# Kernel optimization log

Measured on AMD Instinct MI355X. Metric: run time of the kernel, lower is better.

The kernel has to match this reference:

```python
import jax, jax.numpy as jnp
from jax import lax
import numpy as np

B, T, F_IN, H = 64, 128, 12, 128  # batch, seq_len, input/output features, hidden


def _uinit(key, shape, fan):
    return jax.random.uniform(key, shape, jnp.float32, -1.0, 1.0) / np.float32(np.sqrt(fan))


def setup_inputs() -> dict:
    key = jax.random.key(0)
    ks = jax.random.split(key, 12)
    inp = {
        "x": jax.random.normal(ks[0], (B, T, F_IN), jnp.float32),
        # encoder LSTM (gate order i,f,g,o; b = b_ih + b_hh folded together)
        "enc_Wih": _uinit(ks[1], (4 * H, F_IN), H),
        "enc_Whh": _uinit(ks[2], (4 * H, H), H),
        "enc_b": _uinit(ks[3], (4 * H,), H),
        # decoder LSTM (input is the 12-dim teacher-forced x slice)
        "dec_Wih": _uinit(ks[4], (4 * H, F_IN), H),
        "dec_Whh": _uinit(ks[5], (4 * H, H), H),
        "dec_b": _uinit(ks[6], (4 * H,), H),
        # attention: Linear(2H -> H) with bias, then v: Linear(H -> 1, no bias)
        "attn_W": _uinit(ks[7], (H, 2 * H), 2 * H),
        "attn_b": _uinit(ks[8], (H,), 2 * H),
        "v_w": _uinit(ks[9], (H,), H),
        # output layer: Linear(2H -> F_IN)  (intended width; see notes)
        "out_W": _uinit(ks[10], (F_IN, 2 * H), 2 * H),
        "out_b": _uinit(ks[11], (F_IN,), 2 * H),
    }
    return inp


def _lstm_cell(xt, h, c, Wih, Whh, b):
    z = xt @ Wih.T + h @ Whh.T + b  # [B, 4H]
    i, f, g, o = jnp.split(z, 4, axis=-1)
    c = jax.nn.sigmoid(f) * c + jax.nn.sigmoid(i) * jnp.tanh(g)
    h = jax.nn.sigmoid(o) * jnp.tanh(c)
    return h, c


def reference(x, enc_Wih, enc_Whh, enc_b, dec_Wih, dec_Whh, dec_b,
              attn_W, attn_b, v_w, out_W, out_b):
    b_, t_, _ = x.shape
    hdim = enc_Whh.shape[1]
    xs = jnp.swapaxes(x, 0, 1)  # [T, B, F]
    h0 = jnp.zeros((b_, hdim), x.dtype)
    c0 = jnp.zeros((b_, hdim), x.dtype)

    def enc_step(carry, xt):
        h, c = carry
        h, c = _lstm_cell(xt, h, c, enc_Wih, enc_Whh, enc_b)
        return (h, c), h

    (hT, cT), enc_hs = lax.scan(enc_step, (h0, c0), xs)
    enc_out = jnp.swapaxes(enc_hs, 0, 1)  # [B, T, H]

    # split attn weight: cat(hidden, enc_out) @ W.T == hidden@W1.T + enc_out@W2.T
    W1, W2 = attn_W[:, :hdim], attn_W[:, hdim:]
    enc_proj = jnp.einsum("bth,gh->btg", enc_out, W2)  # precompute encoder side

    def dec_step(carry, xt):
        h, c = carry
        h, c = _lstm_cell(xt, h, c, dec_Wih, dec_Whh, dec_b)
        energy = jnp.tanh((h @ W1.T)[:, None, :] + enc_proj + attn_b)  # [B,T,H]
        score = jnp.einsum("bth,h->bt", energy, v_w)
        w = jax.nn.softmax(score, axis=1)  # attention over encoder time
        ctx = jnp.einsum("bt,bth->bh", w, enc_out)
        return (h, c), jnp.concatenate([h, ctx], axis=-1)  # [B, 2H]

    _, dec_ys = lax.scan(dec_step, (hT, cT), xs)
    dec_out = jnp.swapaxes(dec_ys, 0, 1)  # [B, T, 2H]
    return dec_out @ out_W.T + out_b  # [B, T, F]
```

## Files before the change

kernel.cpp:

```cpp
#include <hip/hip_runtime.h>
#include <hip/hip_bf16.h>

#define BB 64
#define TT 128
#define FIN 12
#define HH 128
#define GG 512

#define LOG2E 1.4426950408889634f
#define TWO_LOG2E 2.8853900817779268f

__device__ __forceinline__ float fexp2(float x) { return __builtin_amdgcn_exp2f(x); }
__device__ __forceinline__ float frcp(float x)  { return __builtin_amdgcn_rcpf(x); }

__device__ __forceinline__ float tanh_f(float x) {
  return 1.0f - 2.0f * frcp(1.0f + fexp2(TWO_LOG2E * x));
}
__device__ __forceinline__ float sigm_f(float x) {
  return frcp(1.0f + fexp2(-LOG2E * x));
}

template <int CTRL>
__device__ __forceinline__ float dpp_addstage(float v) {
  int s = __builtin_amdgcn_update_dpp(0, __float_as_int(v), CTRL, 0xF, 0xF, true);
  return v + __int_as_float(s);
}
__device__ __forceinline__ float red8(float v) {
  v = dpp_addstage<0xB1>(v);
  v = dpp_addstage<0x4E>(v);
  v = dpp_addstage<0x141>(v);
  return v;
}

#define FMA4S(acc, s, v) do { \
  acc.x = fmaf((s), (v).x, acc.x); \
  acc.y = fmaf((s), (v).y, acc.y); \
  acc.z = fmaf((s), (v).z, acc.z); \
  acc.w = fmaf((s), (v).w, acc.w); } while (0)

#define ACC4(hv, wv, a) do { \
  a = fmaf((hv).x, (wv).x, a); a = fmaf((hv).y, (wv).y, a); \
  a = fmaf((hv).z, (wv).z, a); a = fmaf((hv).w, (wv).w, a); } while (0)

__global__ __launch_bounds__(1024, 4) void lstm_kernel(
    const float* __restrict__ x,
    const float* __restrict__ eWih, const float* __restrict__ eWhh, const float* __restrict__ eb,
    const float* __restrict__ dWih, const float* __restrict__ dWhh, const float* __restrict__ db,
    float* __restrict__ encH, float* __restrict__ decH)
{
  const int b   = blockIdx.x;
  const int tid = threadIdx.x;
  const int q   = tid & 7;
  const int i   = tid >> 3;

  __shared__ __align__(16) float xs[TT * FIN];
  __shared__ __align__(16) float hbuf[2][160];
  __shared__ __align__(16) float hist[64 * HH];

  if (tid < (TT * FIN / 4))
    ((float4*)xs)[tid] = ((const float4*)(x + (size_t)b * TT * FIN))[tid];
  if (tid < 320) ((float*)hbuf)[tid] = 0.0f;
  float c = 0.0f;

  const int xo   = (q < 4) ? 3 * q : 0;
  const float xz = (q < 4) ? 1.0f : 0.0f;

  int ts = 0;
  #pragma unroll 1
  for (int phase = 0; phase < 2; ++phase) {
    const float* Wih  = phase ? dWih : eWih;
    const float* Whh  = phase ? dWhh : eWhh;
    const float* bias = phase ? db : eb;
    float* Hout       = phase ? decH : encH;

    float4 wg[4][4];
    #pragma unroll
    for (int g = 0; g < 4; ++g)
      #pragma unroll
      for (int j = 0; j < 4; ++j)
        wg[g][j] = *(const float4*)(Whh + ((g * HH + i) * HH) + 16 * q + 4 * j);

    float wx[4][3];
    #pragma unroll
    for (int g = 0; g < 4; ++g)
      #pragma unroll
      for (int j = 0; j < 3; ++j)
        wx[g][j] = Wih[(g * HH + i) * FIN + xo + j] * xz;

    const float bi = bias[i], bf = bias[HH + i], bg = bias[2 * HH + i], bo = bias[3 * HH + i];

    #pragma unroll 1
    for (int half = 0; half < 2; ++half) {
      #pragma unroll 1
      for (int tt = 0; tt < 64; ++tt, ++ts) {
        const int t = half * 64 + tt;
        __syncthreads();
        const float* hb = hbuf[ts & 1] + q * 20;
        float4 h0 = *(const float4*)(hb + 0);
        float4 h1 = *(const float4*)(hb + 4);
        float4 h2 = *(const float4*)(hb + 8);
        float4 h3 = *(const float4*)(hb + 12);

        const float* xt = xs + t * FIN + xo;
        float x0 = xt[0], x1 = xt[1], x2 = xt[2];
        float ai = wx[0][0] * x0 + wx[0][1] * x1 + wx[0][2] * x2;
        float af = wx[1][0] * x0 + wx[1][1] * x1 + wx[1][2] * x2;
        float ag = wx[2][0] * x0 + wx[2][1] * x1 + wx[2][2] * x2;
        float ao = wx[3][0] * x0 + wx[3][1] * x1 + wx[3][2] * x2;

        ACC4(h0, wg[0][0], ai); ACC4(h0, wg[1][0], af); ACC4(h0, wg[2][0], ag); ACC4(h0, wg[3][0], ao);
        ACC4(h1, wg[0][1], ai); ACC4(h1, wg[1][1], af); ACC4(h1, wg[2][1], ag); ACC4(h1, wg[3][1], ao);
        ACC4(h2, wg[0][2], ai); ACC4(h2, wg[1][2], af); ACC4(h2, wg[2][2], ag); ACC4(h2, wg[3][2], ao);
        ACC4(h3, wg[0][3], ai); ACC4(h3, wg[1][3], af); ACC4(h3, wg[2][3], ag); ACC4(h3, wg[3][3], ao);

        ai = red8(ai); af = red8(af); ag = red8(ag); ao = red8(ao);

        if (q == 0) {
          float zi = sigm_f(ai + bi);
          float zf = sigm_f(af + bf);
          float zg = tanh_f(ag + bg);
          float zo = sigm_f(ao + bo);
          c = fmaf(zf, c, zi * zg);
          float hn = zo * tanh_f(c);
          hbuf[(ts + 1) & 1][(i >> 4) * 20 + (i & 15)] = hn;
          hist[tt * HH + i] = hn;
        }
      }
      __syncthreads();
      {
        float4* dst = (float4*)(Hout + ((size_t)b * TT + half * 64) * HH);
        const float4* src = (const float4*)hist;
        dst[tid]        = src[tid];
        dst[tid + 1024] = src[tid + 1024];
      }
    }
  }
}

__global__ __launch_bounds__(256, 2) void proj_kernel(
    const float* __restrict__ encH, const float* __restrict__ decH,
    const float* __restrict__ attnW, const float* __restrict__ attnb,
    float* __restrict__ Abuf, float* __restrict__ Pbuf)
{
  const int m  = blockIdx.x & 1;
  const int b  = (blockIdx.x >> 1) & 63;
  const int r0 = (blockIdx.x >> 7) * 16;
  const int tid = threadIdx.x;

  __shared__ __align__(16) float WT[64 * 128];
  __shared__ __align__(16) float Xt[16 * 128];

  const float* X = (m ? encH : decH) + ((size_t)b * TT + r0) * HH;
  const float* W = attnW + (m ? HH : 0);

  ((float4*)Xt)[tid]       = ((const float4*)X)[tid];
  ((float4*)Xt)[256 + tid] = ((const float4*)X)[256 + tid];

  const int hq = tid & 31, rr = tid >> 5;
  const int h0 = 4 * hq;

  float4 acc0, acc1;
  if (m == 0) { acc0 = *(const float4*)(attnb + h0); acc1 = acc0; }
  else        { acc0 = make_float4(0.f, 0.f, 0.f, 0.f); acc1 = acc0; }

  for (int kb = 0; kb < 2; ++kb) {
    __syncthreads();
    {
      int h = tid >> 1, koff = (tid & 1) * 32;
      #pragma unroll
      for (int j = 0; j < 8; ++j) {
        float4 v = *(const float4*)(W + h * 256 + kb * 64 + koff + 4 * j);
        int kp = koff + 4 * j;
        WT[(kp + 0) * 128 + h] = v.x;
        WT[(kp + 1) * 128 + h] = v.y;
        WT[(kp + 2) * 128 + h] = v.z;
        WT[(kp + 3) * 128 + h] = v.w;
      }
    }
    __syncthreads();
    const float* xr0 = Xt + (2 * rr) * 128 + kb * 64;
    const float* xr1 = xr0 + 128;
    #pragma unroll
    for (int k4 = 0; k4 < 64; k4 += 4) {
      float4 xa = *(const float4*)(xr0 + k4);
      float4 xb = *(const float4*)(xr1 + k4);
      float4 w0 = *(const float4*)&WT[(k4 + 0) * 128 + h0];
      float4 w1 = *(const float4*)&WT[(k4 + 1) * 128 + h0];
      float4 w2 = *(const float4*)&WT[(k4 + 2) * 128 + h0];
      float4 w3 = *(const float4*)&WT[(k4 + 3) * 128 + h0];
      FMA4S(acc0, xa.x, w0); FMA4S(acc0, xa.y, w1);
      FMA4S(acc0, xa.z, w2); FMA4S(acc0, xa.w, w3);
      FMA4S(acc1, xb.x, w0); FMA4S(acc1, xb.y, w1);
      FMA4S(acc1, xb.z, w2); FMA4S(acc1, xb.w, w3);
    }
  }
  float* O = (m ? Pbuf : Abuf) + ((size_t)b * TT + r0) * HH;
  *(float4*)(O + (2 * rr) * 128 + h0)     = acc0;
  *(float4*)(O + (2 * rr + 1) * 128 + h0) = acc1;
}

#define AST 132

__global__ __launch_bounds__(512, 2) void attn_kernel(
    const float* __restrict__ encH, const float* __restrict__ decH,
    const float* __restrict__ Abuf, const float* __restrict__ Pbuf,
    const float* __restrict__ vw, const float* __restrict__ outW,
    const float* __restrict__ outb, float* __restrict__ out)
{
  const int b  = blockIdx.x >> 3;
  const int s0 = (blockIdx.x & 7) * 16;
  const int tid = threadIdx.x;

  __shared__ __align__(16) float buf[64 * 128];
  __shared__ __align__(16) float a_lds[16 * AST];
  __shared__ __align__(16) float sc[16 * AST];
  __shared__ __align__(16) float dh[16 * 128];
  __shared__ __align__(16) float vl[HH];

  {
    int r = tid >> 5, c4 = (tid & 31) * 4;
    float4 av = *(const float4*)(Abuf + ((size_t)b * TT + s0 + r) * HH + c4);
    av.x = fexp2(TWO_LOG2E * av.x);
    av.y = fexp2(TWO_LOG2E * av.y);
    av.z = fexp2(TWO_LOG2E * av.z);
    av.w = fexp2(TWO_LOG2E * av.w);
    *(float4*)&a_lds[r * AST + c4] = av;
  }
  ((float4*)dh)[tid] = ((const float4*)(decH + ((size_t)b * TT + s0) * HH))[tid];
  if (tid < 32) ((float4*)vl)[tid] = ((const float4*)vw)[tid];

  const int u  = tid & 31;
  const int sl = tid >> 5;
  const int uq = u & 15;
  const int uh = u >> 4;

  for (int half = 0; half < 2; ++half) {
    const int tbase = half * 64;
    __syncthreads();
    #pragma unroll
    for (int i = 0; i < 4; ++i) {
      int flat = i * 2048 + tid * 4;
      int tp = flat >> 7;
      int h0 = flat & 127;
      float4 v = *(const float4*)(Pbuf + ((size_t)b * TT + tbase + tp) * HH + h0);
      v.x = fexp2(TWO_LOG2E * v.x);
      v.y = fexp2(TWO_LOG2E * v.y);
      v.z = fexp2(TWO_LOG2E * v.z);
      v.w = fexp2(TWO_LOG2E * v.w);
      int tq = tp >> 2, tr = tp & 3;
      buf[(h0 + 0) * 64 + 4 * ((tq ^ ((h0 + 0) >> 2)) & 15) + tr] = v.x;
      buf[(h0 + 1) * 64 + 4 * ((tq ^ ((h0 + 1) >> 2)) & 15) + tr] = v.y;
      buf[(h0 + 2) * 64 + 4 * ((tq ^ ((h0 + 2) >> 2)) & 15) + tr] = v.z;
      buf[(h0 + 3) * 64 + 4 * ((tq ^ ((h0 + 3) >> 2)) & 15) + tr] = v.w;
    }
    __syncthreads();
    float4 acc = make_float4(0.f, 0.f, 0.f, 0.f);
    const float* earow = a_lds + sl * AST;
    #pragma unroll 4
    for (int hh = 0; hh < 64; hh += 4) {
      const int h = uh * 64 + hh;
      float4 ea = *(const float4*)&earow[h];
      float4 va = *(const float4*)&vl[h];
      const int xoff = 4 * ((uq ^ ((h >> 2) & 15)) & 15);
      float4 p0 = *(const float4*)&buf[(h + 0) * 64 + xoff];
      float4 p1 = *(const float4*)&buf[(h + 1) * 64 + xoff];
      float4 p2 = *(const float4*)&buf[(h + 2) * 64 + xoff];
      float4 p3 = *(const float4*)&buf[(h + 3) * 64 + xoff];
      acc.x = fmaf(va.x, frcp(fmaf(ea.x, p0.x, 1.f)), acc.x);
      acc.y = fmaf(va.x, frcp(fmaf(ea.x, p0.y, 1.f)), acc.y);
      acc.z = fmaf(va.x, frcp(fmaf(ea.x, p0.z, 1.f)), acc.z);
      acc.w = fmaf(va.x, frcp(fmaf(ea.x, p0.w, 1.f)), acc.w);
      acc.x = fmaf(va.y, frcp(fmaf(ea.y, p1.x, 1.f)), acc.x);
      acc.y = fmaf(va.y, frcp(fmaf(ea.y, p1.y, 1.f)), acc.y);
      acc.z = fmaf(va.y, frcp(fmaf(ea.y, p1.z, 1.f)), acc.z);
      acc.w = fmaf(va.y, frcp(fmaf(ea.y, p1.w, 1.f)), acc.w);
      acc.x = fmaf(va.z, frcp(fmaf(ea.z, p2.x, 1.f)), acc.x);
      acc.y = fmaf(va.z, frcp(fmaf(ea.z, p2.y, 1.f)), acc.y);
      acc.z = fmaf(va.z, frcp(fmaf(ea.z, p2.z, 1.f)), acc.z);
      acc.w = fmaf(va.z, frcp(fmaf(ea.z, p2.w, 1.f)), acc.w);
      acc.x = fmaf(va.w, frcp(fmaf(ea.w, p3.x, 1.f)), acc.x);
      acc.y = fmaf(va.w, frcp(fmaf(ea.w, p3.y, 1.f)), acc.y);
      acc.z = fmaf(va.w, frcp(fmaf(ea.w, p3.z, 1.f)), acc.z);
      acc.w = fmaf(va.w, frcp(fmaf(ea.w, p3.w, 1.f)), acc.w);
    }
    acc.x += __shfl_xor(acc.x, 16, 64);
    acc.y += __shfl_xor(acc.y, 16, 64);
    acc.z += __shfl_xor(acc.z, 16, 64);
    acc.w += __shfl_xor(acc.w, 16, 64);
    if (uh == 0) {
      float4 o;
      o.x = -2.f * acc.x; o.y = -2.f * acc.y;
      o.z = -2.f * acc.z; o.w = -2.f * acc.w;
      *(float4*)&sc[sl * AST + tbase + 4 * uq] = o;
    }
  }
  __syncthreads();

  {
    float4 sv = *(const float4*)&sc[sl * AST + 4 * u];
    float mx = fmaxf(fmaxf(sv.x, sv.y), fmaxf(sv.z, sv.w));
    #pragma unroll
    for (int msk = 1; msk <= 16; msk <<= 1) mx = fmaxf(mx, __shfl_xor(mx, msk, 64));
    float4 e;
    e.x = fexp2(LOG2E * (sv.x - mx));
    e.y = fexp2(LOG2E * (sv.y - mx));
    e.z = fexp2(LOG2E * (sv.z - mx));
    e.w = fexp2(LOG2E * (sv.w - mx));
    float sm = (e.x + e.y) + (e.z + e.w);
    #pragma unroll
    for (int msk = 1; msk <= 16; msk <<= 1) sm += __shfl_xor(sm, msk, 64);
    float r = frcp(sm);
    e.x *= r; e.y *= r; e.z *= r; e.w *= r;
    *(float4*)&sc[sl * AST + 4 * u] = e;
  }

  float4 ctx = make_float4(0.f, 0.f, 0.f, 0.f);
  const int h0c = 4 * u;
  for (int half = 0; half < 2; ++half) {
    const int tbase = half * 64;
    __syncthreads();
    #pragma unroll
    for (int i = 0; i < 4; ++i) {
      int flat = i * 2048 + tid * 4;
      int tp = flat >> 7;
      int hh0 = flat & 127;
      *(float4*)&buf[tp * 128 + hh0] =
          *(const float4*)(encH + ((size_t)b * TT + tbase + tp) * HH + hh0);
    }
    __syncthreads();
    const float* wrow = sc + sl * AST + tbase;
    #pragma unroll 8
    for (int tp = 0; tp < 64; ++tp) {
      float wt = wrow[tp];
      float4 e4 = *(const float4*)&buf[tp * 128 + h0c];
      FMA4S(ctx, wt, e4);
    }
  }
  __syncthreads();
  *(float4*)&a_lds[sl * AST + h0c] = ctx;
  __syncthreads();

  if (tid < 192) {
    int s = tid / 12, f = tid % 12;
    float acc = outb[f];
    const float4* w4 = (const float4*)(outW + f * 256);
    const float4* d4 = (const float4*)(dh + s * 128);
    const float4* c4 = (const float4*)(a_lds + s * AST);
    #pragma unroll
    for (int k = 0; k < 32; ++k) {
      float4 wv = w4[k], dv = d4[k];
      acc = fmaf(wv.x, dv.x, acc); acc = fmaf(wv.y, dv.y, acc);
      acc = fmaf(wv.z, dv.z, acc); acc = fmaf(wv.w, dv.w, acc);
    }
    #pragma unroll
    for (int k = 0; k < 32; ++k) {
      float4 wv = w4[32 + k], cv = c4[k];
      acc = fmaf(wv.x, cv.x, acc); acc = fmaf(wv.y, cv.y, acc);
      acc = fmaf(wv.z, cv.z, acc); acc = fmaf(wv.w, cv.w, acc);
    }
    out[((size_t)b * TT + s0 + s) * FIN + f] = acc;
  }
}

extern "C" void kernel_launch(void* const* d_in, const int* in_sizes, int n_in,
                              void* d_out, int out_size, void* d_ws, size_t ws_size,
                              hipStream_t stream)
{
  const float* x     = (const float*)d_in[0];
  const float* eWih  = (const float*)d_in[1];
  const float* eWhh  = (const float*)d_in[2];
  const float* eb    = (const float*)d_in[3];
  const float* dWih  = (const float*)d_in[4];
  const float* dWhh  = (const float*)d_in[5];
  const float* db    = (const float*)d_in[6];
  const float* attnW = (const float*)d_in[7];
  const float* attnb = (const float*)d_in[8];
  const float* vw    = (const float*)d_in[9];
  const float* outW  = (const float*)d_in[10];
  const float* outb  = (const float*)d_in[11];
  float* out = (float*)d_out;

  float* ws   = (float*)d_ws;
  const size_t SEG = (size_t)BB * TT * HH;
  float* encH = ws;
  float* decH = ws + SEG;
  float* Abuf = ws + 2 * SEG;
  float* Pbuf = ws + 3 * SEG;

  lstm_kernel<<<64, 1024, 0, stream>>>(x, eWih, eWhh, eb, dWih, dWhh, db, encH, decH);
  proj_kernel<<<1024, 256, 0, stream>>>(encH, decH, attnW, attnb, Abuf, Pbuf);
  attn_kernel<<<512, 512, 0, stream>>>(encH, decH, Abuf, Pbuf, vw, outW, outb, out);
}
```

Baseline: 322.3 us.

## Split LSTM into encoder/decoder kernels and overlap encoder projection with decoder

The fused LSTM kernel is split into an encoder kernel and a decoder kernel. The decoder kernel launches extra blocks that compute the encoder-side attention projection (with the exp pre-applied) while the 64 decoder blocks run their serial recurrence, which should hide the projection work behind the recurrent phase. The decoder-side projection moves into the attention kernel, computed per tile straight from global weights, so the separate proj kernel and the Abuf round trip go away. Costs are an extra kernel launch, encoder state passed through global memory, and redundant weight reads in the attention kernel.

```diff
diff --git a/kernel.cpp b/kernel.cpp
--- a/kernel.cpp
+++ b/kernel.cpp
@@ -5,7 +5,6 @@
 #define TT 128
 #define FIN 12
 #define HH 128
-#define GG 512
 
 #define LOG2E 1.4426950408889634f
 #define TWO_LOG2E 2.8853900817779268f
@@ -42,11 +41,83 @@
   a = fmaf((hv).x, (wv).x, a); a = fmaf((hv).y, (wv).y, a); \
   a = fmaf((hv).z, (wv).z, a); a = fmaf((hv).w, (wv).w, a); } while (0)
 
-__global__ __launch_bounds__(1024, 4) void lstm_kernel(
+__device__ __forceinline__ void lstm_phase(
+    const float* __restrict__ Wih, const float* __restrict__ Whh,
+    const float* __restrict__ bias, float* __restrict__ Hout ,
+    float* __restrict__ xs, float (*hbuf)[160], float* __restrict__ hist,
+    const int tid, const int q, const int i, float& c)
+{
+  const int xo   = (q < 4) ? 3 * q : 0;
+  const float xz = (q < 4) ? 1.0f : 0.0f;
+
+  float4 wg[4][4];
+  #pragma unroll
+  for (int g = 0; g < 4; ++g)
+    #pragma unroll
+    for (int j = 0; j < 4; ++j)
+      wg[g][j] = *(const float4*)(Whh + ((g * HH + i) * HH) + 16 * q + 4 * j);
+
+  float wx[4][3];
+  #pragma unroll
+  for (int g = 0; g < 4; ++g)
+    #pragma unroll
+    for (int j = 0; j < 3; ++j)
+      wx[g][j] = Wih[(g * HH + i) * FIN + xo + j] * xz;
+
+  const float bi = bias[i], bf = bias[HH + i], bg = bias[2 * HH + i], bo = bias[3 * HH + i];
+
+  int ts = 0;
+  #pragma unroll 1
+  for (int half = 0; half < 2; ++half) {
+    #pragma unroll 1
+    for (int tt = 0; tt < 64; ++tt, ++ts) {
+      const int t = half * 64 + tt;
+      __syncthreads();
+      const float* hb = (const float*)hbuf[ts & 1] + q * 20;
+      float4 h0 = *(const float4*)(hb + 0);
+      float4 h1 = *(const float4*)(hb + 4);
+      float4 h2 = *(const float4*)(hb + 8);
+      float4 h3 = *(const float4*)(hb + 12);
+
+      const float* xt = xs + t * FIN + xo;
+      float x0 = xt[0], x1 = xt[1], x2 = xt[2];
+      float ai = wx[0][0] * x0 + wx[0][1] * x1 + wx[0][2] * x2;
+      float af = wx[1][0] * x0 + wx[1][1] * x1 + wx[1][2] * x2;
+      float ag = wx[2][0] * x0 + wx[2][1] * x1 + wx[2][2] * x2;
+      float ao = wx[3][0] * x0 + wx[3][1] * x1 + wx[3][2] * x2;
+
+      ACC4(h0, wg[0][0], ai); ACC4(h0, wg[1][0], af); ACC4(h0, wg[2][0], ag); ACC4(h0, wg[3][0], ao);
+      ACC4(h1, wg[0][1], ai); ACC4(h1, wg[1][1], af); ACC4(h1, wg[2][1], ag); ACC4(h1, wg[3][1], ao);
+      ACC4(h2, wg[0][2], ai); ACC4(h2, wg[1][2], af); ACC4(h2, wg[2][2], ag); ACC4(h2, wg[3][2], ao);
+      ACC4(h3, wg[0][3], ai); ACC4(h3, wg[1][3], af); ACC4(h3, wg[2][3], ag); ACC4(h3, wg[3][3], ao);
+
+      ai = red8(ai); af = red8(af); ag = red8(ag); ao = red8(ao);
+
+      if (q == 0) {
+        float zi = sigm_f(ai + bi);
+        float zf = sigm_f(af + bf);
+        float zg = tanh_f(ag + bg);
+        float zo = sigm_f(ao + bo);
+        c = fmaf(zf, c, zi * zg);
+        float hn = zo * tanh_f(c);
+        hbuf[(ts + 1) & 1][(i >> 4) * 20 + (i & 15)] = hn;
+        hist[tt * HH + i] = hn;
+      }
+    }
+    __syncthreads();
+    {
+      float4* dst = (float4*)(Hout + (size_t)(half * 64) * HH);
+      const float4* src = (const float4*)hist;
+      dst[tid]        = src[tid];
+      dst[tid + 1024] = src[tid + 1024];
+    }
+  }
+}
+
+__global__ __launch_bounds__(1024, 4) void lstm_enc_kernel(
     const float* __restrict__ x,
     const float* __restrict__ eWih, const float* __restrict__ eWhh, const float* __restrict__ eb,
-    const float* __restrict__ dWih, const float* __restrict__ dWhh, const float* __restrict__ db,
-    float* __restrict__ encH, float* __restrict__ decH)
+    float* __restrict__ encH, float* __restrict__ cbuf)
 {
   const int b   = blockIdx.x;
   const int tid = threadIdx.x;
@@ -62,148 +133,101 @@
   if (tid < 320) ((float*)hbuf)[tid] = 0.0f;
   float c = 0.0f;
 
-  const int xo   = (q < 4) ? 3 * q : 0;
-  const float xz = (q < 4) ? 1.0f : 0.0f;
-
-  int ts = 0;
-  #pragma unroll 1
-  for (int phase = 0; phase < 2; ++phase) {
-    const float* Wih  = phase ? dWih : eWih;
-    const float* Whh  = phase ? dWhh : eWhh;
-    const float* bias = phase ? db : eb;
-    float* Hout       = phase ? decH : encH;
-
-    float4 wg[4][4];
-    #pragma unroll
-    for (int g = 0; g < 4; ++g)
-      #pragma unroll
-      for (int j = 0; j < 4; ++j)
-        wg[g][j] = *(const float4*)(Whh + ((g * HH + i) * HH) + 16 * q + 4 * j);
-
-    float wx[4][3];
-    #pragma unroll
-    for (int g = 0; g < 4; ++g)
-      #pragma unroll
-      for (int j = 0; j < 3; ++j)
-        wx[g][j] = Wih[(g * HH + i) * FIN + xo + j] * xz;
-
-    const float bi = bias[i], bf = bias[HH + i], bg = bias[2 * HH + i], bo = bias[3 * HH + i];
+  lstm_phase(eWih, eWhh, eb, encH + (size_t)b * TT * HH, xs, hbuf, hist, tid, q, i, c);
+
+  if (q == 0) cbuf[b * HH + i] = c;
+}
+
+__global__ __launch_bounds__(1024, 4) void lstm_dec_p_kernel(
+    const float* __restrict__ x,
+    const float* __restrict__ dWih, const float* __restrict__ dWhh, const float* __restrict__ db,
+    const float* __restrict__ attnW,
+    const float* __restrict__ encH, const float* __restrict__ cbuf,
+    float* __restrict__ decH, float* __restrict__ Pbuf)
+{
+  __shared__ __align__(16) float smem[12416];
+  const int tid = threadIdx.x;
+
+  if (blockIdx.x < 64) {
+    const int b = blockIdx.x;
+    const int q = tid & 7;
+    const int i = tid >> 3;
+    float* xs           = smem;
+    float (*hbuf)[160]  = (float(*)[160])(smem + 1536);
+    float* hist         = smem + 1856;
+
+    if (tid < (TT * FIN / 4))
+      ((float4*)xs)[tid] = ((const float4*)(x + (size_t)b * TT * FIN))[tid];
+    if (tid < 128) {
+      float hv = encH[((size_t)b * TT + 127) * HH + tid];
+      hbuf[0][(tid >> 4) * 20 + (tid & 15)] = hv;
+    }
+    float c = 0.0f;
+    if (q == 0) c = cbuf[b * HH + i];
+
+    lstm_phase(dWih, dWhh, db, decH + (size_t)b * TT * HH, xs, hbuf, hist, tid, q, i, c);
+  } else {
+    const int pb = blockIdx.x - 64;
+    const int b  = pb & 63;
+    const int r0 = (pb >> 6) * 64;
+    float* WT = smem;
+    float* Xt = smem + 4224;
+
+    const float* X = encH + ((size_t)b * TT + r0) * HH;
+    ((float4*)Xt)[tid]        = ((const float4*)X)[tid];
+    ((float4*)Xt)[tid + 1024] = ((const float4*)X)[tid + 1024];
+
+    const float* W = attnW + HH;
+    const int hq = tid & 31, rr = tid >> 5;
+    const int h0 = 4 * hq;
+
+    float4 acc0 = make_float4(0.f, 0.f, 0.f, 0.f);
+    float4 acc1 = acc0;
 
     #pragma unroll 1
-    for (int half = 0; half < 2; ++half) {
-      #pragma unroll 1
-      for (int tt = 0; tt < 64; ++tt, ++ts) {
-        const int t = half * 64 + tt;
-        __syncthreads();
-        const float* hb = hbuf[ts & 1] + q * 20;
-        float4 h0 = *(const float4*)(hb + 0);
-        float4 h1 = *(const float4*)(hb + 4);
-        float4 h2 = *(const float4*)(hb + 8);
-        float4 h3 = *(const float4*)(hb + 12);
-
-        const float* xt = xs + t * FIN + xo;
-        float x0 = xt[0], x1 = xt[1], x2 = xt[2];
-        float ai = wx[0][0] * x0 + wx[0][1] * x1 + wx[0][2] * x2;
-        float af = wx[1][0] * x0 + wx[1][1] * x1 + wx[1][2] * x2;
-        float ag = wx[2][0] * x0 + wx[2][1] * x1 + wx[2][2] * x2;
-        float ao = wx[3][0] * x0 + wx[3][1] * x1 + wx[3][2] * x2;
-
-        ACC4(h0, wg[0][0], ai); ACC4(h0, wg[1][0], af); ACC4(h0, wg[2][0], ag); ACC4(h0, wg[3][0], ao);
-        ACC4(h1, wg[0][1], ai); ACC4(h1, wg[1][1], af); ACC4(h1, wg[2][1], ag); ACC4(h1, wg[3][1], ao);
-        ACC4(h2, wg[0][2], ai); ACC4(h2, wg[1][2], af); ACC4(h2, wg[2][2], ag); ACC4(h2, wg[3][2], ao);
-        ACC4(h3, wg[0][3], ai); ACC4(h3, wg[1][3], af); ACC4(h3, wg[2][3], ag); ACC4(h3, wg[3][3], ao);
-
-        ai = red8(ai); af = red8(af); ag = red8(ag); ao = red8(ao);
-
-        if (q == 0) {
-          float zi = sigm_f(ai + bi);
-          float zf = sigm_f(af + bf);
-          float zg = tanh_f(ag + bg);
-          float zo = sigm_f(ao + bo);
-          c = fmaf(zf, c, zi * zg);
-          float hn = zo * tanh_f(c);
-          hbuf[(ts + 1) & 1][(i >> 4) * 20 + (i & 15)] = hn;
-          hist[tt * HH + i] = hn;
-        }
+    for (int kb = 0; kb < 4; ++kb) {
+      __syncthreads();
+      {
+        int h = tid >> 3, koff = (tid & 7) * 4;
+        float4 v = *(const float4*)(W + h * 256 + kb * 32 + koff);
+        WT[(koff + 0) * 132 + h] = v.x;
+        WT[(koff + 1) * 132 + h] = v.y;
+        WT[(koff + 2) * 132 + h] = v.z;
+        WT[(koff + 3) * 132 + h] = v.w;
       }
       __syncthreads();
-      {
-        float4* dst = (float4*)(Hout + ((size_t)b * TT + half * 64) * HH);
-        const float4* src = (const float4*)hist;
-        dst[tid]        = src[tid];
-        dst[tid + 1024] = src[tid + 1024];
+      const float* xr0 = Xt + (2 * rr) * 128 + kb * 32;
+      const float* xr1 = xr0 + 128;
+      #pragma unroll
+      for (int k4 = 0; k4 < 32; k4 += 4) {
+        float4 xa = *(const float4*)(xr0 + k4);
+        float4 xb = *(const float4*)(xr1 + k4);
+        float4 w0 = *(const float4*)&WT[(k4 + 0) * 132 + h0];
+        float4 w1 = *(const float4*)&WT[(k4 + 1) * 132 + h0];
+        float4 w2 = *(const float4*)&WT[(k4 + 2) * 132 + h0];
+        float4 w3 = *(const float4*)&WT[(k4 + 3) * 132 + h0];
+        FMA4S(acc0, xa.x, w0); FMA4S(acc0, xa.y, w1);
+        FMA4S(acc0, xa.z, w2); FMA4S(acc0, xa.w, w3);
+        FMA4S(acc1, xb.x, w0); FMA4S(acc1, xb.y, w1);
+        FMA4S(acc1, xb.z, w2); FMA4S(acc1, xb.w, w3);
       }
     }
-  }
-}
-
-__global__ __launch_bounds__(256, 2) void proj_kernel(
-    const float* __restrict__ encH, const float* __restrict__ decH,
-    const float* __restrict__ attnW, const float* __restrict__ attnb,
-    float* __restrict__ Abuf, float* __restrict__ Pbuf)
-{
-  const int m  = blockIdx.x & 1;
-  const int b  = (blockIdx.x >> 1) & 63;
-  const int r0 = (blockIdx.x >> 7) * 16;
-  const int tid = threadIdx.x;
-
-  __shared__ __align__(16) float WT[64 * 128];
-  __shared__ __align__(16) float Xt[16 * 128];
-
-  const float* X = (m ? encH : decH) + ((size_t)b * TT + r0) * HH;
-  const float* W = attnW + (m ? HH : 0);
-
-  ((float4*)Xt)[tid]       = ((const float4*)X)[tid];
-  ((float4*)Xt)[256 + tid] = ((const float4*)X)[256 + tid];
-
-  const int hq = tid & 31, rr = tid >> 5;
-  const int h0 = 4 * hq;
-
-  float4 acc0, acc1;
-  if (m == 0) { acc0 = *(const float4*)(attnb + h0); acc1 = acc0; }
-  else        { acc0 = make_float4(0.f, 0.f, 0.f, 0.f); acc1 = acc0; }
-
-  for (int kb = 0; kb < 2; ++kb) {
-    __syncthreads();
-    {
-      int h = tid >> 1, koff = (tid & 1) * 32;
-      #pragma unroll
-      for (int j = 0; j < 8; ++j) {
-        float4 v = *(const float4*)(W + h * 256 + kb * 64 + koff + 4 * j);
-        int kp = koff + 4 * j;
-        WT[(kp + 0) * 128 + h] = v.x;
-        WT[(kp + 1) * 128 + h] = v.y;
-        WT[(kp + 2) * 128 + h] = v.z;
-        WT[(kp + 3) * 128 + h] = v.w;
-      }
-    }
-    __syncthreads();
-    const float* xr0 = Xt + (2 * rr) * 128 + kb * 64;
-    const float* xr1 = xr0 + 128;
-    #pragma unroll
-    for (int k4 = 0; k4 < 64; k4 += 4) {
-      float4 xa = *(const float4*)(xr0 + k4);
-      float4 xb = *(const float4*)(xr1 + k4);
-      float4 w0 = *(const float4*)&WT[(k4 + 0) * 128 + h0];
-      float4 w1 = *(const float4*)&WT[(k4 + 1) * 128 + h0];
-      float4 w2 = *(const float4*)&WT[(k4 + 2) * 128 + h0];
-      float4 w3 = *(const float4*)&WT[(k4 + 3) * 128 + h0];
-      FMA4S(acc0, xa.x, w0); FMA4S(acc0, xa.y, w1);
-      FMA4S(acc0, xa.z, w2); FMA4S(acc0, xa.w, w3);
-      FMA4S(acc1, xb.x, w0); FMA4S(acc1, xb.y, w1);
-      FMA4S(acc1, xb.z, w2); FMA4S(acc1, xb.w, w3);
-    }
-  }
-  float* O = (m ? Pbuf : Abuf) + ((size_t)b * TT + r0) * HH;
-  *(float4*)(O + (2 * rr) * 128 + h0)     = acc0;
-  *(float4*)(O + (2 * rr + 1) * 128 + h0) = acc1;
+    acc0.x = fexp2(TWO_LOG2E * acc0.x); acc0.y = fexp2(TWO_LOG2E * acc0.y);
+    acc0.z = fexp2(TWO_LOG2E * acc0.z); acc0.w = fexp2(TWO_LOG2E * acc0.w);
+    acc1.x = fexp2(TWO_LOG2E * acc1.x); acc1.y = fexp2(TWO_LOG2E * acc1.y);
+    acc1.z = fexp2(TWO_LOG2E * acc1.z); acc1.w = fexp2(TWO_LOG2E * acc1.w);
+    float* O = Pbuf + ((size_t)b * TT + r0) * HH;
+    *(float4*)(O + (2 * rr) * 128 + h0)     = acc0;
+    *(float4*)(O + (2 * rr + 1) * 128 + h0) = acc1;
+  }
 }
 
 #define AST 132
 
 __global__ __launch_bounds__(512, 2) void attn_kernel(
     const float* __restrict__ encH, const float* __restrict__ decH,
-    const float* __restrict__ Abuf, const float* __restrict__ Pbuf,
+    const float* __restrict__ Pbuf,
+    const float* __restrict__ attnW, const float* __restrict__ attnb,
     const float* __restrict__ vw, const float* __restrict__ outW,
     const float* __restrict__ outb, float* __restrict__ out)
 {
@@ -217,15 +241,6 @@
   __shared__ __align__(16) float dh[16 * 128];
   __shared__ __align__(16) float vl[HH];
 
-  {
-    int r = tid >> 5, c4 = (tid & 31) * 4;
-    float4 av = *(const float4*)(Abuf + ((size_t)b * TT + s0 + r) * HH + c4);
-    av.x = fexp2(TWO_LOG2E * av.x);
-    av.y = fexp2(TWO_LOG2E * av.y);
-    av.z = fexp2(TWO_LOG2E * av.z);
-    av.w = fexp2(TWO_LOG2E * av.w);
-    *(float4*)&a_lds[r * AST + c4] = av;
-  }
   ((float4*)dh)[tid] = ((const float4*)(decH + ((size_t)b * TT + s0) * HH))[tid];
   if (tid < 32) ((float4*)vl)[tid] = ((const float4*)vw)[tid];
 
@@ -233,6 +248,35 @@
   const int sl = tid >> 5;
   const int uq = u & 15;
   const int uh = u >> 4;
+
+  __syncthreads();
+
+  {
+    const int h0 = 4 * u;
+    float4 acc = *(const float4*)(attnb + h0);
+    const float* drow = dh + sl * 128;
+    const float* w0p = attnW + (size_t)(h0 + 0) * 256;
+    const float* w1p = attnW + (size_t)(h0 + 1) * 256;
+    const float* w2p = attnW + (size_t)(h0 + 2) * 256;
+    const float* w3p = attnW + (size_t)(h0 + 3) * 256;
+    #pragma unroll 8
+    for (int k4 = 0; k4 < 128; k4 += 4) {
+      float4 dv = *(const float4*)(drow + k4);
+      float4 wa = *(const float4*)(w0p + k4);
+      float4 wb = *(const float4*)(w1p + k4);
+      float4 wc = *(const float4*)(w2p + k4);
+      float4 wd = *(const float4*)(w3p + k4);
+      ACC4(dv, wa, acc.x);
+      ACC4(dv, wb, acc.y);
+      ACC4(dv, wc, acc.z);
+      ACC4(dv, wd, acc.w);
+    }
+    acc.x = fexp2(TWO_LOG2E * acc.x);
+    acc.y = fexp2(TWO_LOG2E * acc.y);
+    acc.z = fexp2(TWO_LOG2E * acc.z);
+    acc.w = fexp2(TWO_LOG2E * acc.w);
+    *(float4*)&a_lds[sl * AST + h0] = acc;
+  }
 
   for (int half = 0; half < 2; ++half) {
     const int tbase = half * 64;
@@ -243,10 +287,6 @@
       int tp = flat >> 7;
       int h0 = flat & 127;
       float4 v = *(const float4*)(Pbuf + ((size_t)b * TT + tbase + tp) * HH + h0);
-      v.x = fexp2(TWO_LOG2E * v.x);
-      v.y = fexp2(TWO_LOG2E * v.y);
-      v.z = fexp2(TWO_LOG2E * v.z);
-      v.w = fexp2(TWO_LOG2E * v.w);
       int tq = tp >> 2, tr = tp & 3;
       buf[(h0 + 0) * 64 + 4 * ((tq ^ ((h0 + 0) >> 2)) & 15) + tr] = v.x;
       buf[(h0 + 1) * 64 + 4 * ((tq ^ ((h0 + 1) >> 2)) & 15) + tr] = v.y;
@@ -384,10 +424,10 @@
   const size_t SEG = (size_t)BB * TT * HH;
   float* encH = ws;
   float* decH = ws + SEG;
-  float* Abuf = ws + 2 * SEG;
-  float* Pbuf = ws + 3 * SEG;
-
-  lstm_kernel<<<64, 1024, 0, stream>>>(x, eWih, eWhh, eb, dWih, dWhh, db, encH, decH);
-  proj_kernel<<<1024, 256, 0, stream>>>(encH, decH, attnW, attnb, Abuf, Pbuf);
-  attn_kernel<<<512, 512, 0, stream>>>(encH, decH, Abuf, Pbuf, vw, outW, outb, out);
-}
+  float* Pbuf = ws + 2 * SEG;
+  float* cbuf = ws + 3 * SEG;
+
+  lstm_enc_kernel<<<64, 1024, 0, stream>>>(x, eWih, eWhh, eb, encH, cbuf);
+  lstm_dec_p_kernel<<<192, 1024, 0, stream>>>(x, dWih, dWhh, db, attnW, encH, cbuf, decH, Pbuf);
+  attn_kernel<<<512, 512, 0, stream>>>(encH, decH, Pbuf, attnW, attnb, vw, outW, outb, out);
+}
```

Measured after the change: 364.8 us. 13.2% more time.
